# Performance work log

Measured on AMD Instinct MI355X. Metric: run time of the kernel, lower is better.

The kernel has to match this reference:

```python
import jax, jax.numpy as jnp
import numpy as np

B, S, D, H = 1, 2048, 4096, 32
HD = D // H  # 128


def setup_inputs() -> dict:
    key = jax.random.key(0)
    ks = jax.random.split(key, 6)
    x = jax.random.normal(ks[0], (B, S, D), dtype=jnp.float32)
    # rotary angles: standard llama freqs, position * inv_freq
    inv_freq = 1.0 / (10000.0 ** (jnp.arange(0, HD, 2, dtype=jnp.float32) / HD))  # (HD/2,)
    freqs = jnp.arange(S, dtype=jnp.float32)[:, None] * inv_freq[None, :]  # (S, HD/2)
    scale = 0.02
    wq = jax.random.normal(ks[1], (D, D), dtype=jnp.float32) * scale
    wk = jax.random.normal(ks[2], (D, D), dtype=jnp.float32) * scale
    wv = jax.random.normal(ks[3], (D, D), dtype=jnp.float32) * scale
    wo = jax.random.normal(ks[4], (D, D), dtype=jnp.float32) * scale
    return {"x": x, "freqs": freqs, "wq": wq, "wk": wk, "wv": wv, "wo": wo}


def _rope(t, cos, sin):
    # t: (B,S,H,HD); pairs are interleaved (complex view of last dim)
    b, s, h, d = t.shape
    t2 = t.reshape(b, s, h, d // 2, 2)
    t0, t1 = t2[..., 0], t2[..., 1]
    o0 = t0 * cos - t1 * sin
    o1 = t0 * sin + t1 * cos
    return jnp.stack([o0, o1], axis=-1).reshape(b, s, h, d)


def reference(x, freqs, wq, wk, wv, wo):
    b, s, d = x.shape
    hd = 2 * freqs.shape[-1]
    h = d // hd
    # projections (torch Linear: y = x @ W.T)
    q = (x @ wq.T).reshape(b, s, h, hd)
    k = (x @ wk.T).reshape(b, s, h, hd)
    v = (x @ wv.T).reshape(b, s, h, hd)
    cos = jnp.cos(freqs)[None, :s, None, :]  # (1,S,1,HD/2)
    sin = jnp.sin(freqs)[None, :s, None, :]
    q = _rope(q, cos, sin)
    k = _rope(k, cos, sin)
    q = q.transpose(0, 2, 1, 3)  # (B,H,S,HD)
    k = k.transpose(0, 2, 1, 3)
    v = v.transpose(0, 2, 1, 3)
    scale = jnp.sqrt(jnp.float32(hd))
    scores = jnp.einsum('bhqd,bhkd->bhqk', q, k).astype(jnp.float32) / scale
    # causal mask (qp == ep path): -inf strictly above diagonal
    mask = jnp.triu(jnp.full((s, s), -jnp.inf, dtype=scores.dtype), k=1)
    scores = scores + mask[None, None]
    attn = jax.nn.softmax(scores, axis=-1).astype(q.dtype)
    out = jnp.einsum('bhqk,bhkd->bhqd', attn, v)
    out = out.transpose(0, 2, 1, 3).reshape(b, s, d)
    return out @ wo.T
```

## Files before the change

kernel.cpp:

```cpp
#include <hip/hip_runtime.h>
#include <hip/hip_bf16.h>
#include <stdint.h>


typedef __attribute__((ext_vector_type(8))) short bf16x8;
typedef __attribute__((ext_vector_type(4))) float f32x4;

#define S_LEN 2048
#define DMODEL 4096
#define NHEAD 32
#define HDIM 128
#define QKV_LD 12288

__device__ __forceinline__ unsigned short f2bf(float f) {
  unsigned int u = __float_as_uint(f);
  unsigned int r = u + 0x7FFFu + ((u >> 16) & 1u);
  return (unsigned short)(r >> 16);
}
__device__ __forceinline__ float bf2f(unsigned short h) {
  return __uint_as_float(((unsigned int)h) << 16);
}
__device__ __forceinline__ void gl_lds16(const void* g, void* l) {
  __builtin_amdgcn_global_load_lds((const __attribute__((address_space(1))) unsigned int*)g,
                                   (__attribute__((address_space(3))) unsigned int*)l, 16, 0, 0);
}
__device__ __forceinline__ void phase_barrier() {
  __builtin_amdgcn_sched_barrier(0);
  asm volatile("" ::: "memory");
  __builtin_amdgcn_s_barrier();
  asm volatile("" ::: "memory");
  __builtin_amdgcn_sched_barrier(0);
}
__device__ __forceinline__ void wait_vmcnt6() {
  __builtin_amdgcn_sched_barrier(0);
  asm volatile("s_waitcnt vmcnt(6)" ::: "memory");
  __builtin_amdgcn_sched_barrier(0);
}
__device__ __forceinline__ void wait_vmcnt4() {
  __builtin_amdgcn_sched_barrier(0);
  asm volatile("s_waitcnt vmcnt(4)" ::: "memory");
  __builtin_amdgcn_sched_barrier(0);
}

__device__ __forceinline__ void cvt4(const float* __restrict__ s, unsigned short* __restrict__ d,
                                     int i) {
  float4 v = ((const float4*)s)[i];
  ushort4 o;
  o.x = f2bf(v.x); o.y = f2bf(v.y); o.z = f2bf(v.z); o.w = f2bf(v.w);
  ((ushort4*)d)[i] = o;
}

__global__ __launch_bounds__(256) void prep_inputs(const float* __restrict__ x,
                                                   const float* __restrict__ wq,
                                                   const float* __restrict__ wk,
                                                   const float* __restrict__ wv,
                                                   const float* __restrict__ wo,
                                                   const float* __restrict__ fr,
                                                   unsigned short* __restrict__ xb,
                                                   unsigned short* __restrict__ wqkvb,
                                                   unsigned short* __restrict__ wob,
                                                   float* __restrict__ cs) {
  const int NX = 2097152;
  const int NW = 4194304;
  const int NR = S_LEN * 64;
  const int total = NX + 4 * NW + NR;
  int i = blockIdx.x * blockDim.x + threadIdx.x;
  int stride = gridDim.x * blockDim.x;
  for (; i < total; i += stride) {
    if (i < NX) {
      cvt4(x, xb, i);
    } else if (i < NX + NW) {
      cvt4(wq, wqkvb, i - NX);
    } else if (i < NX + 2 * NW) {
      cvt4(wk, wqkvb + 16777216, i - NX - NW);
    } else if (i < NX + 3 * NW) {
      cvt4(wv, wqkvb + 33554432, i - NX - 2 * NW);
    } else if (i < NX + 4 * NW) {
      cvt4(wo, wob, i - NX - 3 * NW);
    } else {
      int j = i - (NX + 4 * NW);
      float f = fr[j];
      cs[2 * j]     = cosf(f);
      cs[2 * j + 1] = sinf(f);
    }
  }
}

__device__ __forceinline__ void mfma_quad(f32x4 (&acc)[8][4], const bf16x8 (&af)[4][2],
                                          const bf16x8 (&bf)[2][2], int moff, int noff) {
  __builtin_amdgcn_s_setprio(1);
#pragma unroll
  for (int mi = 0; mi < 4; ++mi)
#pragma unroll
    for (int ni = 0; ni < 2; ++ni)
#pragma unroll
      for (int kk = 0; kk < 2; ++kk)
        acc[moff + mi][noff + ni] = __builtin_amdgcn_mfma_f32_16x16x32_bf16(
            af[mi][kk], bf[ni][kk], acc[moff + mi][noff + ni], 0, 0, 0);
  __builtin_amdgcn_s_setprio(0);
}
__device__ __forceinline__ void mfma_quad2(f32x4 (&acc)[4][4], const bf16x8 (&af)[2][2],
                                           const bf16x8 (&bf)[2][2], int moff, int noff) {
  __builtin_amdgcn_s_setprio(1);
#pragma unroll
  for (int mi = 0; mi < 2; ++mi)
#pragma unroll
    for (int ni = 0; ni < 2; ++ni)
#pragma unroll
      for (int kk = 0; kk < 2; ++kk)
        acc[moff + mi][noff + ni] = __builtin_amdgcn_mfma_f32_16x16x32_bf16(
            af[mi][kk], bf[ni][kk], acc[moff + mi][noff + ni], 0, 0, 0);
  __builtin_amdgcn_s_setprio(0);
}

__device__ __forceinline__ void read_a(bf16x8 (&dst)[4][2], const char* base, int half,
                                       int wr, int l15, int l4, int swz) {
#pragma unroll
  for (int mi = 0; mi < 4; ++mi) {
    const char* rb = base + (wr * 128 + half * 64 + mi * 16 + l15) * 128;
#pragma unroll
    for (int kk = 0; kk < 2; ++kk)
      dst[mi][kk] = *(const bf16x8*)(rb + ((kk * 64 + l4 * 16) ^ swz));
  }
}
__device__ __forceinline__ void read_b(bf16x8 (&dst)[2][2], const char* base, int half,
                                       int wc, int l15, int l4, int swz) {
#pragma unroll
  for (int ni = 0; ni < 2; ++ni) {
    const char* rb = base + (wc * 64 + half * 32 + ni * 16 + l15) * 128;
#pragma unroll
    for (int kk = 0; kk < 2; ++kk)
      dst[ni][kk] = *(const bf16x8*)(rb + ((kk * 64 + l4 * 16) ^ swz));
  }
}
__device__ __forceinline__ void read_a2(bf16x8 (&dst)[2][2], const char* base, int half,
                                        int wr, int l15, int l4, int swz) {
#pragma unroll
  for (int mi = 0; mi < 2; ++mi) {
    const char* rb = base + (wr * 64 + half * 32 + mi * 16 + l15) * 128;
#pragma unroll
    for (int kk = 0; kk < 2; ++kk)
      dst[mi][kk] = *(const bf16x8*)(rb + ((kk * 64 + l4 * 16) ^ swz));
  }
}
__device__ __forceinline__ void read_b2(bf16x8 (&dst)[2][2], const char* base, int half,
                                        int wc, int l15, int l4, int swz) {
#pragma unroll
  for (int ni = 0; ni < 2; ++ni) {
    const char* rb = base + (wc * 64 + half * 32 + ni * 16 + l15) * 128;
#pragma unroll
    for (int kk = 0; kk < 2; ++kk)
      dst[ni][kk] = *(const bf16x8*)(rb + ((kk * 64 + l4 * 16) ^ swz));
  }
}

template <bool OUT_BF16, bool ROPE>
__device__ __forceinline__ void gemm256_body(const unsigned short* __restrict__ A,
                                             const unsigned short* __restrict__ B,
                                             void* __restrict__ C,
                                             int M, int N, int K, int ldc,
                                             char* smem, int wg,
                                             const float* __restrict__ cs) {
  const int tid = threadIdx.x;
  const int lane = tid & 63, wid = tid >> 6;
  const int wr = wid >> 2, wc = wid & 3;
  const int l15 = lane & 15, l4 = lane >> 4;

  const int nbn = N >> 8;
  const int bm = wg / nbn, bn = wg % nbn;
  const int nk = K >> 6;

  unsigned short* AlB = (unsigned short*)smem;
  unsigned short* BlB = (unsigned short*)smem + 32768;

  const int srow = tid >> 3;
  const int scol = ((tid & 7) ^ (srow & 7)) * 8;
  const unsigned short* Asrc = A + (size_t)(bm * 256 + srow) * K + scol;
  const unsigned short* Bsrc = B + (size_t)(bn * 256 + srow) * K + scol;
  const int ldsdst = wid * 512;

#define STA(b, kt, q) gl_lds16(Asrc + ((size_t)(q) * 64) * K + (kt) * 64, AlB + (b) * 16384 + (q) * 4096 + ldsdst)
#define STB(b, kt, q) gl_lds16(Bsrc + ((size_t)(q) * 64) * K + (kt) * 64, BlB + (b) * 16384 + (q) * 4096 + ldsdst)

  const int swz = (l15 & 7) << 4;

  f32x4 acc[8][4] = {};
  bf16x8 Ax[4][2], Ay[4][2], B0f[2][2], B1f[2][2];

#pragma unroll
  for (int q = 0; q < 4; ++q) STA(0, 0, q);
#pragma unroll
  for (int q = 0; q < 4; ++q) STB(0, 0, q);
  {
    const int k1 = (nk > 1) ? 1 : 0;
    STA(1, k1, 0); STA(1, k1, 2);
    STB(1, k1, 0); STB(1, k1, 1); STB(1, k1, 2); STB(1, k1, 3);
  }
  wait_vmcnt6();
  phase_barrier();
  read_a(Ax, (const char*)AlB, 0, wr, l15, l4, swz);
  read_b(B0f, (const char*)BlB, 0, wc, l15, l4, swz);

#define HALF(bb, AC, AA, t)                                                \
  {                                                                        \
    const int kt1 = ((t) + 1 < nk) ? (t) + 1 : nk - 1;                     \
    const int kt2 = ((t) + 2 < nk) ? (t) + 2 : nk - 1;                     \
    const char* Ab = (const char*)(AlB + (bb) * 16384);                    \
    const char* Bb = (const char*)(BlB + (bb) * 16384);                    \
    const char* Abn = (const char*)(AlB + ((bb) ^ 1) * 16384);             \
    const char* Bbn = (const char*)(BlB + ((bb) ^ 1) * 16384);             \
    STA((bb) ^ 1, kt1, 1); STA((bb) ^ 1, kt1, 3);                          \
    phase_barrier();                                                       \
    mfma_quad(acc, AC, B0f, 0, 0);                                 \
    read_a(AA, Ab, 1, wr, l15, l4, swz);                                   \
    STA(bb, kt2, 0); STA(bb, kt2, 2);                                      \
    phase_barrier();                                                       \
    mfma_quad(acc, AA, B0f, 4, 0);                                 \
    read_b(B1f, Bb, 1, wc, l15, l4, swz);                                  \
    STB(bb, kt2, 0); STB(bb, kt2, 1);                                      \
    phase_barrier();                                                       \
    mfma_quad(acc, AA, B1f, 4, 2);                                 \
    STB(bb, kt2, 2); STB(bb, kt2, 3);                                      \
    wait_vmcnt6();                                                         \
    phase_barrier();                                                       \
    mfma_quad(acc, AC, B1f, 0, 2);                                 \
    read_a(AA, Abn, 0, wr, l15, l4, swz);                                  \
    read_b(B0f, Bbn, 0, wc, l15, l4, swz);                                 \
  }

  for (int t = 0; t < nk; t += 2) {
    HALF(0, Ax, Ay, t);
    HALF(1, Ay, Ax, t + 1);
  }
#undef HALF
#undef STA
#undef STB

  __builtin_amdgcn_sched_barrier(0);
  asm volatile("s_waitcnt vmcnt(0)" ::: "memory");

  const size_t crow0 = (size_t)bm * 256 + wr * 128 + l4 * 4;
  const int ccol0 = bn * 256 + wc * 64 + l15;
#pragma unroll
  for (int mf = 0; mf < 8; ++mf)
#pragma unroll
    for (int nf = 0; nf < 4; ++nf) {
      size_t row = crow0 + mf * 16;
      int col = ccol0 + nf * 16;
      if (ROPE) {
        const int d = col & (HDIM - 1);
        const int i2 = d & ~1;
        unsigned short* Cp = (unsigned short*)C;
#pragma unroll
        for (int r = 0; r < 4; ++r) {
          float v = acc[mf][nf][r];
          float vp = __shfl_xor(v, 1, 64);
          float2 csv = *(const float2*)&cs[(row + r) * HDIM + i2];
          float o = ((d & 1) == 0) ? (v * csv.x - vp * csv.y)
                                   : (vp * csv.y + v * csv.x);
          Cp[(row + r) * ldc + col] = f2bf(o);
        }
      } else if (OUT_BF16) {
        unsigned short* Cp = (unsigned short*)C;
#pragma unroll
        for (int r = 0; r < 4; ++r) Cp[(row + r) * ldc + col] = f2bf(acc[mf][nf][r]);
      } else {
        float* Cp = (float*)C;
#pragma unroll
        for (int r = 0; r < 4; ++r) Cp[(row + r) * ldc + col] = acc[mf][nf][r];
      }
    }
}

template <bool OUT_BF16>
__device__ __forceinline__ void gemm128_body(const unsigned short* __restrict__ A,
                                             const unsigned short* __restrict__ B,
                                             void* __restrict__ C,
                                             int M, int N, int K, int ldc,
                                             char* smem, int wg) {
  const int tid = threadIdx.x;
  const int lane = tid & 63, wid = tid >> 6;
  const int wr = wid >> 2, wc = wid & 3;
  const int l15 = lane & 15, l4 = lane >> 4;

  const int nbn = N >> 8;
  const int bm = wg / nbn, bn = wg % nbn;
  const int nk = K >> 6;

  unsigned short* AlB = (unsigned short*)smem;
  unsigned short* BlB = (unsigned short*)smem + 16384;

  const int srow = tid >> 3;
  const int scol = ((tid & 7) ^ (srow & 7)) * 8;
  const unsigned short* Asrc = A + (size_t)(bm * 128 + srow) * K + scol;
  const unsigned short* Bsrc = B + (size_t)(bn * 256 + srow) * K + scol;
  const int ldsdst = wid * 512;

#define STA2(b, kt, q) gl_lds16(Asrc + ((size_t)(q) * 64) * K + (kt) * 64, AlB + (b) * 8192 + (q) * 4096 + ldsdst)
#define STB2(b, kt, q) gl_lds16(Bsrc + ((size_t)(q) * 64) * K + (kt) * 64, BlB + (b) * 16384 + (q) * 4096 + ldsdst)

  const int swz = (l15 & 7) << 4;

  f32x4 acc[4][4] = {};
  bf16x8 Ax[2][2], Ay[2][2], B0f[2][2], B1f[2][2];

  STA2(0, 0, 0); STA2(0, 0, 1);
#pragma unroll
  for (int q = 0; q < 4; ++q) STB2(0, 0, q);
  {
    const int k1 = (nk > 1) ? 1 : 0;
    STA2(1, k1, 0); STA2(1, k1, 1);
    STB2(1, k1, 0); STB2(1, k1, 1);
  }
  wait_vmcnt4();
  phase_barrier();
  read_a2(Ax, (const char*)AlB, 0, wr, l15, l4, swz);
  read_b2(B0f, (const char*)BlB, 0, wc, l15, l4, swz);

#define HALF2(bb, AC, AA, t)                                               \
  {                                                                        \
    const int kt1 = ((t) + 1 < nk) ? (t) + 1 : nk - 1;                     \
    const int kt2 = ((t) + 2 < nk) ? (t) + 2 : nk - 1;                     \
    const char* Ab = (const char*)(AlB + (bb) * 8192);                     \
    const char* Bb = (const char*)(BlB + (bb) * 16384);                    \
    const char* Abn = (const char*)(AlB + ((bb) ^ 1) * 8192);              \
    const char* Bbn = (const char*)(BlB + ((bb) ^ 1) * 16384);             \
    STB2((bb) ^ 1, kt1, 2); STB2((bb) ^ 1, kt1, 3);        \
    phase_barrier();                                                       \
    mfma_quad2(acc, AC, B0f, 0, 0);                                \
    read_a2(AA, Ab, 1, wr, l15, l4, swz);                                  \
    STA2(bb, kt2, 0); STA2(bb, kt2, 1);                                    \
    phase_barrier();                                                       \
    mfma_quad2(acc, AA, B0f, 2, 0);                                \
    read_b2(B1f, Bb, 1, wc, l15, l4, swz);                                 \
    STB2(bb, kt2, 0); STB2(bb, kt2, 1);                                    \
    phase_barrier();                                                       \
    mfma_quad2(acc, AA, B1f, 2, 2);                                \
    wait_vmcnt4();                                                         \
    phase_barrier();                                                       \
    mfma_quad2(acc, AC, B1f, 0, 2);                                \
    read_a2(AA, Abn, 0, wr, l15, l4, swz);                                 \
    read_b2(B0f, Bbn, 0, wc, l15, l4, swz);                                \
  }

  for (int t = 0; t < nk; t += 2) {
    HALF2(0, Ax, Ay, t);
    HALF2(1, Ay, Ax, t + 1);
  }
#undef HALF2
#undef STA2
#undef STB2

  __builtin_amdgcn_sched_barrier(0);
  asm volatile("s_waitcnt vmcnt(0)" ::: "memory");

  const size_t crow0 = (size_t)bm * 128 + wr * 64 + l4 * 4;
  const int ccol0 = bn * 256 + wc * 64 + l15;
#pragma unroll
  for (int mf = 0; mf < 4; ++mf)
#pragma unroll
    for (int nf = 0; nf < 4; ++nf) {
      size_t row = crow0 + mf * 16;
      int col = ccol0 + nf * 16;
      if (OUT_BF16) {
        unsigned short* Cp = (unsigned short*)C;
#pragma unroll
        for (int r = 0; r < 4; ++r) Cp[(row + r) * ldc + col] = f2bf(acc[mf][nf][r]);
      } else {
        float* Cp = (float*)C;
#pragma unroll
        for (int r = 0; r < 4; ++r) Cp[(row + r) * ldc + col] = acc[mf][nf][r];
      }
    }
}

__global__ __launch_bounds__(512, 2) void qkv_proj(const unsigned short* __restrict__ xb,
                                                   const unsigned short* __restrict__ wqkvb,
                                                   unsigned short* __restrict__ qkvb,
                                                   const float* __restrict__ cs) {
  __shared__ __align__(16) char smem[131072];
  const int b = blockIdx.x;
  if (b < 256) {
    gemm256_body<true, true>(xb, wqkvb, qkvb, 2048, 8192, 4096, QKV_LD, smem, b, cs);
  } else {
    gemm128_body<true>(xb, wqkvb + 33554432, qkvb + 8192, 2048, 4096, 4096, QKV_LD, smem, b - 256);
  }
}

__global__ __launch_bounds__(512, 2) void out_proj(const unsigned short* __restrict__ A,
                                                   const unsigned short* __restrict__ B,
                                                   float* __restrict__ C) {
  __shared__ __align__(16) char smem[98304];
  gemm128_body<false>(A, B, C, 2048, 4096, 4096, 4096, smem, blockIdx.x);
}

__global__ __launch_bounds__(256) void v_transpose(const unsigned short* __restrict__ qkv,
                                                   unsigned short* __restrict__ vt) {
  __shared__ unsigned short T[64][68];
  int sb = blockIdx.x * 64;
  int h = blockIdx.y >> 1;
  int d0 = (blockIdx.y & 1) * 64;
  int tid = threadIdx.x;
#pragma unroll
  for (int i = 0; i < 2; ++i) {
    int b = i * 256 + tid;
    int r = b >> 3, c = b & 7;
    const ushort4* src = (const ushort4*)(qkv + (size_t)(sb + r) * QKV_LD + 8192 + h * HDIM + d0 + c * 8);
    ushort4 a0 = src[0], a1 = src[1];
    *(ushort4*)&T[r][c * 8] = a0;
    *(ushort4*)&T[r][c * 8 + 4] = a1;
  }
  __syncthreads();
#pragma unroll
  for (int i = 0; i < 2; ++i) {
    int b = i * 256 + tid;
    int dd = b >> 3, sc = b & 7;
    unsigned short tmp[8];
#pragma unroll
    for (int j = 0; j < 8; ++j) tmp[j] = T[sc * 8 + j][dd];
    unsigned short* dst = vt + (size_t)(h * HDIM + d0 + dd) * S_LEN + sb + sc * 8;
    ushort4 lo = make_ushort4(tmp[0], tmp[1], tmp[2], tmp[3]);
    ushort4 hi = make_ushort4(tmp[4], tmp[5], tmp[6], tmp[7]);
    *(ushort4*)dst = lo;
    *(ushort4*)(dst + 4) = hi;
  }
}

__global__ __launch_bounds__(256) void attn_kernel(const unsigned short* __restrict__ qkv,
                                                   const unsigned short* __restrict__ vt,
                                                   float* __restrict__ pacc,
                                                   float* __restrict__ pm,
                                                   float* __restrict__ pl) {
  __shared__ __align__(16) unsigned short Klds[64 * 128];
  __shared__ __align__(16) unsigned short Vtlds[128 * 64];
  __shared__ __align__(16) unsigned short Plds[4][16 * 64];
  const int tid = threadIdx.x, lane = tid & 63, w = tid >> 6;
  const int l15 = lane & 15, l4 = lane >> 4;
  const int h = blockIdx.x & 31;
  const int jj = blockIdx.x >> 5;

  int bq, c, kt0, kt1;
  if (jj < 17) {
    bq = 31 - jj; c = 0; kt0 = 0; kt1 = 16;
  } else {
    int k = jj - 17;
    if (k == 0)      { bq = 31;            c = 1; }
    else if (k & 1)  { bq = 30 - (k >> 1); c = 1; }
    else             { bq = 15 - (k >> 1); c = 0; }
    kt0 = c ? 16 : 0;
    kt1 = bq + 1;
  }
  const int qw = bq * 64 + w * 16;

  bf16x8 qf[4];
#pragma unroll
  for (int ds = 0; ds < 4; ++ds)
    qf[ds] = *(const bf16x8*)&qkv[(size_t)(qw + l15) * QKV_LD + h * HDIM + ds * 32 + l4 * 8];

  f32x4 acc[8] = {};
  float m_run[4], l_run[4];
#pragma unroll
  for (int r = 0; r < 4; ++r) { m_run[r] = -1e30f; l_run[r] = 0.f; }

  const float scale = 0.08838834764831845f;
  for (int kt = kt0; kt < kt1; ++kt) {
    const int kv0 = kt * 64;
    __syncthreads();
#pragma unroll
    for (int i = 0; i < 4; ++i) {
      int b = (w * 4 + i) * 64 + lane;
      int r = b >> 4, cc = b & 15;
      gl_lds16(qkv + (size_t)(kv0 + r) * QKV_LD + 4096 + h * HDIM + ((cc ^ (r & 15)) * 8),
               &Klds[(w * 4 + i) * 512]);
    }
#pragma unroll
    for (int i = 0; i < 4; ++i) {
      int b = (w * 4 + i) * 64 + lane;
      int r = b >> 3, cc = b & 7;
      gl_lds16(vt + (size_t)(h * HDIM + r) * S_LEN + kv0 + ((cc ^ (r & 7)) * 8),
               &Vtlds[(w * 4 + i) * 512]);
    }
    __syncthreads();

    f32x4 s[4] = {};
#pragma unroll
    for (int jt = 0; jt < 4; ++jt) {
      int kr = jt * 16 + l15;
#pragma unroll
      for (int ds = 0; ds < 4; ++ds) {
        int cc = (ds * 4 + l4) ^ (kr & 15);
        bf16x8 kf = *(const bf16x8*)&Klds[kr * 128 + cc * 8];
        s[jt] = __builtin_amdgcn_mfma_f32_16x16x32_bf16(qf[ds], kf, s[jt], 0, 0, 0);
      }
    }

    const bool diag = (kt == bq);
#pragma unroll
    for (int jt = 0; jt < 4; ++jt)
#pragma unroll
      for (int r = 0; r < 4; ++r) {
        float v = s[jt][r] * scale;
        if (diag) {
          int kvg = kv0 + jt * 16 + l15;
          int qg = qw + l4 * 4 + r;
          if (kvg > qg) v = -1e30f;
        }
        s[jt][r] = v;
      }

    float alpha[4];
#pragma unroll
    for (int r = 0; r < 4; ++r) {
      float mx = fmaxf(fmaxf(s[0][r], s[1][r]), fmaxf(s[2][r], s[3][r]));
#pragma unroll
      for (int off = 1; off < 16; off <<= 1) mx = fmaxf(mx, __shfl_xor(mx, off, 64));
      float mi = fmaxf(m_run[r], mx);
      alpha[r] = __expf(m_run[r] - mi);
      m_run[r] = mi;
      float sum = 0.f;
#pragma unroll
      for (int jt = 0; jt < 4; ++jt) {
        float p = __expf(s[jt][r] - mi);
        s[jt][r] = p;
        sum += p;
      }
#pragma unroll
      for (int off = 1; off < 16; off <<= 1) sum += __shfl_xor(sum, off, 64);
      l_run[r] = l_run[r] * alpha[r] + sum;
    }
#pragma unroll
    for (int dt = 0; dt < 8; ++dt)
#pragma unroll
      for (int r = 0; r < 4; ++r) acc[dt][r] *= alpha[r];

    unsigned short* P = &Plds[w][0];
#pragma unroll
    for (int jt = 0; jt < 4; ++jt)
#pragma unroll
      for (int r = 0; r < 4; ++r) {
        int row = l4 * 4 + r, col = jt * 16 + l15;
        P[(row * 64 + col) ^ ((row & 7) << 3)] = f2bf(s[jt][r]);
      }

#pragma unroll
    for (int ks = 0; ks < 2; ++ks) {
      bf16x8 pa = *(const bf16x8*)&P[(l15 * 64 + ks * 32 + l4 * 8) ^ ((l15 & 7) << 3)];
#pragma unroll
      for (int dt = 0; dt < 8; ++dt) {
        int vr = dt * 16 + l15;
        int cc = (ks * 4 + l4) ^ (vr & 7);
        bf16x8 vf = *(const bf16x8*)&Vtlds[vr * 64 + cc * 8];
        acc[dt] = __builtin_amdgcn_mfma_f32_16x16x32_bf16(pa, vf, acc[dt], 0, 0, 0);
      }
    }
  }

  const size_t bj = ((size_t)h * 32 + bq) * 2 + c;
  float* pa = pacc + bj * 8192 + (size_t)(w * 16) * 128;
#pragma unroll
  for (int dt = 0; dt < 8; ++dt)
#pragma unroll
    for (int r = 0; r < 4; ++r)
      pa[(l4 * 4 + r) * 128 + dt * 16 + l15] = acc[dt][r];
  if (l15 == 0) {
#pragma unroll
    for (int r = 0; r < 4; ++r) {
      pm[bj * 64 + w * 16 + l4 * 4 + r] = m_run[r];
      pl[bj * 64 + w * 16 + l4 * 4 + r] = l_run[r];
    }
  }
}

__global__ __launch_bounds__(256) void attn_combine(const float* __restrict__ pacc,
                                                    const float* __restrict__ pm,
                                                    const float* __restrict__ pl,
                                                    unsigned short* __restrict__ out) {
  const int x = blockIdx.x;
  const int bq = x >> 5, h = x & 31;
  const int tid = threadIdx.x;
  const int row = tid >> 2;
  const int d0 = (tid & 3) * 32;
  const size_t base = ((size_t)h * 32 + bq) * 2;
  const float m0 = pm[base * 64 + row];
  const float l0 = pl[base * 64 + row];
  const int nc = (bq >= 16) ? 2 : 1;
  float w0 = 1.f, w1 = 0.f, denom = l0;
  if (nc == 2) {
    float m1 = pm[(base + 1) * 64 + row];
    float l1 = pl[(base + 1) * 64 + row];
    float M = fmaxf(m0, m1);
    w0 = __expf(m0 - M);
    w1 = __expf(m1 - M);
    denom = w0 * l0 + w1 * l1;
  }
  const float inv = 1.f / denom;
  const float* a0 = pacc + base * 8192 + row * 128 + d0;
  const float* a1 = a0 + 8192;
  unsigned short* op = out + (size_t)(bq * 64 + row) * DMODEL + h * HDIM + d0;
#pragma unroll
  for (int i = 0; i < 8; ++i) {
    float4 v = *(const float4*)(a0 + i * 4);
    v.x *= w0; v.y *= w0; v.z *= w0; v.w *= w0;
    if (nc == 2) {
      float4 u = *(const float4*)(a1 + i * 4);
      v.x += w1 * u.x; v.y += w1 * u.y; v.z += w1 * u.z; v.w += w1 * u.w;
    }
    ushort4 o;
    o.x = f2bf(v.x * inv); o.y = f2bf(v.y * inv);
    o.z = f2bf(v.z * inv); o.w = f2bf(v.w * inv);
    *(ushort4*)(op + i * 4) = o;
  }
}

extern "C" void kernel_launch(void* const* d_in, const int* in_sizes, int n_in,
                              void* d_out, int out_size, void* d_ws, size_t ws_size,
                              hipStream_t stream) {
  const float* x = (const float*)d_in[0];
  const float* fr = (const float*)d_in[1];
  const float* wq = (const float*)d_in[2];
  const float* wk = (const float*)d_in[3];
  const float* wv = (const float*)d_in[4];
  const float* wo = (const float*)d_in[5];

  char* ws = (char*)d_ws;
  const size_t OFF_XB   = 0;
  const size_t OFF_WQKV = 16777216;
  const size_t OFF_WO   = OFF_WQKV + 100663296;
  const size_t OFF_QKV  = OFF_WO + 33554432;
  const size_t OFF_CS   = OFF_QKV + 50331648;
  const size_t OFF_VT   = OFF_CS + 1048576;
  const size_t OFF_ATTN = OFF_VT + 16777216;

  unsigned short* xb    = (unsigned short*)(ws + OFF_XB);
  unsigned short* wqkvb = (unsigned short*)(ws + OFF_WQKV);
  unsigned short* wob   = (unsigned short*)(ws + OFF_WO);
  unsigned short* qkvb  = (unsigned short*)(ws + OFF_QKV);
  float*          cs    = (float*)(ws + OFF_CS);
  unsigned short* vt    = (unsigned short*)(ws + OFF_VT);
  unsigned short* attn  = (unsigned short*)(ws + OFF_ATTN);
  float* pacc = (float*)(ws + OFF_WQKV);
  float* pm   = (float*)(ws + OFF_WQKV + 67108864);
  float* pl   = (float*)(ws + OFF_WQKV + 67633152);

  prep_inputs<<<2048, 256, 0, stream>>>(x, wq, wk, wv, wo, fr, xb, wqkvb, wob, cs);
  qkv_proj<<<dim3(512), 512, 0, stream>>>(xb, wqkvb, qkvb, cs);
  v_transpose<<<dim3(32, 64), 256, 0, stream>>>(qkvb, vt);
  attn_kernel<<<dim3(1536), 256, 0, stream>>>(qkvb, vt, pacc, pm, pl);
  attn_combine<<<dim3(1024), 256, 0, stream>>>(pacc, pm, pl, attn);
  out_proj<<<dim3(256), 512, 0, stream>>>(attn, wob, (float*)d_out);
}
```

Before: 477.6 us.

## Double-buffer K/V tiles in attention with async prefetch two tiles ahead

Splits the K and Vt shared-memory tiles into two buffers and issues the global-to-LDS loads for tile kt+2 right after finishing compute on tile kt. The loop now waits with vmcnt(8) instead of two full __syncthreads, so load latency can overlap with the MFMA work. This doubles LDS use to about 72KB per block, which may reduce occupancy, and at the end of the range it issues redundant loads of the last tile.

Result: no change. 480.0 us (+0.5%).

```diff
diff --git a/kernel.cpp b/kernel.cpp
--- a/kernel.cpp
+++ b/kernel.cpp
@@ -39,6 +39,11 @@
 __device__ __forceinline__ void wait_vmcnt4() {
   __builtin_amdgcn_sched_barrier(0);
   asm volatile("s_waitcnt vmcnt(4)" ::: "memory");
+  __builtin_amdgcn_sched_barrier(0);
+}
+__device__ __forceinline__ void wait_vmcnt8() {
+  __builtin_amdgcn_sched_barrier(0);
+  asm volatile("s_waitcnt vmcnt(8)" ::: "memory");
   __builtin_amdgcn_sched_barrier(0);
 }
 
@@ -431,8 +436,8 @@
                                                    float* __restrict__ pacc,
                                                    float* __restrict__ pm,
                                                    float* __restrict__ pl) {
-  __shared__ __align__(16) unsigned short Klds[64 * 128];
-  __shared__ __align__(16) unsigned short Vtlds[128 * 64];
+  __shared__ __align__(16) unsigned short Klds[2][64 * 128];
+  __shared__ __align__(16) unsigned short Vtlds[2][128 * 64];
   __shared__ __align__(16) unsigned short Plds[4][16 * 64];
   const int tid = threadIdx.x, lane = tid & 63, w = tid >> 6;
   const int l15 = lane & 15, l4 = lane >> 4;
@@ -462,25 +467,36 @@
 #pragma unroll
   for (int r = 0; r < 4; ++r) { m_run[r] = -1e30f; l_run[r] = 0.f; }
 
+#define STAGE_KV(kt, bi)                                                            \
+  {                                                                                 \
+    const int kv0s = (kt) * 64;                                                     \
+    _Pragma("unroll") for (int i = 0; i < 4; ++i) {                                 \
+      int b2 = (w * 4 + i) * 64 + lane;                                             \
+      int r = b2 >> 4, cc = b2 & 15;                                                \
+      gl_lds16(qkv + (size_t)(kv0s + r) * QKV_LD + 4096 + h * HDIM +                \
+                   ((cc ^ (r & 15)) * 8),                                           \
+               &Klds[bi][(w * 4 + i) * 512]);                                       \
+    }                                                                               \
+    _Pragma("unroll") for (int i = 0; i < 4; ++i) {                                 \
+      int b2 = (w * 4 + i) * 64 + lane;                                             \
+      int r = b2 >> 3, cc = b2 & 7;                                                 \
+      gl_lds16(vt + (size_t)(h * HDIM + r) * S_LEN + kv0s + ((cc ^ (r & 7)) * 8),   \
+               &Vtlds[bi][(w * 4 + i) * 512]);                                      \
+    }                                                                               \
+  }
+
   const float scale = 0.08838834764831845f;
+  STAGE_KV(kt0, 0);
+  {
+    const int t1 = (kt0 + 1 < kt1) ? kt0 + 1 : kt1 - 1;
+    STAGE_KV(t1, 1);
+  }
+
   for (int kt = kt0; kt < kt1; ++kt) {
+    const int bufi = (kt - kt0) & 1;
     const int kv0 = kt * 64;
-    __syncthreads();
-#pragma unroll
-    for (int i = 0; i < 4; ++i) {
-      int b = (w * 4 + i) * 64 + lane;
-      int r = b >> 4, cc = b & 15;
-      gl_lds16(qkv + (size_t)(kv0 + r) * QKV_LD + 4096 + h * HDIM + ((cc ^ (r & 15)) * 8),
-               &Klds[(w * 4 + i) * 512]);
-    }
-#pragma unroll
-    for (int i = 0; i < 4; ++i) {
-      int b = (w * 4 + i) * 64 + lane;
-      int r = b >> 3, cc = b & 7;
-      gl_lds16(vt + (size_t)(h * HDIM + r) * S_LEN + kv0 + ((cc ^ (r & 7)) * 8),
-               &Vtlds[(w * 4 + i) * 512]);
-    }
-    __syncthreads();
+    wait_vmcnt8();
+    phase_barrier();
 
     f32x4 s[4] = {};
 #pragma unroll
@@ -489,7 +505,7 @@
 #pragma unroll
       for (int ds = 0; ds < 4; ++ds) {
         int cc = (ds * 4 + l4) ^ (kr & 15);
-        bf16x8 kf = *(const bf16x8*)&Klds[kr * 128 + cc * 8];
+        bf16x8 kf = *(const bf16x8*)&Klds[bufi][kr * 128 + cc * 8];
         s[jt] = __builtin_amdgcn_mfma_f32_16x16x32_bf16(qf[ds], kf, s[jt], 0, 0, 0);
       }
     }
@@ -549,11 +565,18 @@
       for (int dt = 0; dt < 8; ++dt) {
         int vr = dt * 16 + l15;
         int cc = (ks * 4 + l4) ^ (vr & 7);
-        bf16x8 vf = *(const bf16x8*)&Vtlds[vr * 64 + cc * 8];
+        bf16x8 vf = *(const bf16x8*)&Vtlds[bufi][vr * 64 + cc * 8];
         acc[dt] = __builtin_amdgcn_mfma_f32_16x16x32_bf16(pa, vf, acc[dt], 0, 0, 0);
       }
     }
-  }
+
+    phase_barrier();
+    {
+      const int tn = (kt + 2 < kt1) ? kt + 2 : kt1 - 1;
+      STAGE_KV(tn, bufi);
+    }
+  }
+#undef STAGE_KV
 
   const size_t bj = ((size_t)h * 32 + bq) * 2 + c;
   float* pa = pacc + bj * 8192 + (size_t)(w * 16) * 128;
```

## Fuse V transpose into QKV GEMM epilogue, fold softmax scale, skip combine for unsplit rows

Applied to the files above, without the earlier changes.

The V projection GEMM now writes its output already transposed through a shared-memory staging tile, which removes the separate v_transpose kernel and its extra round trip of V through global memory. The softmax scale times log2(e) is folded into Q during the RoPE epilogue, so attention uses exp2 and drops the per-score multiply. Query blocks that are not split across two KV chunks write their normalised output directly, so the combine kernel runs only on the split half and launches half as many blocks. The transpose epilogue adds LDS traffic and a barrier to the GEMM, and the folded scale slightly changes the rounding of Q in bf16.

After: 414.4 us. 1.15x faster.

```diff
diff --git a/kernel.cpp b/kernel.cpp
--- a/kernel.cpp
+++ b/kernel.cpp
@@ -11,6 +11,8 @@
 #define NHEAD 32
 #define HDIM 128
 #define QKV_LD 12288
+
+#define QSCALE 0.1275247584969759f
 
 __device__ __forceinline__ unsigned short f2bf(float f) {
   unsigned int u = __float_as_uint(f);
@@ -250,6 +252,7 @@
       if (ROPE) {
         const int d = col & (HDIM - 1);
         const int i2 = d & ~1;
+        const float fs = (col < 4096) ? QSCALE : 1.0f;
         unsigned short* Cp = (unsigned short*)C;
 #pragma unroll
         for (int r = 0; r < 4; ++r) {
@@ -258,7 +261,7 @@
           float2 csv = *(const float2*)&cs[(row + r) * HDIM + i2];
           float o = ((d & 1) == 0) ? (v * csv.x - vp * csv.y)
                                    : (vp * csv.y + v * csv.x);
-          Cp[(row + r) * ldc + col] = f2bf(o);
+          Cp[(row + r) * ldc + col] = f2bf(o * fs);
         }
       } else if (OUT_BF16) {
         unsigned short* Cp = (unsigned short*)C;
@@ -272,7 +275,7 @@
     }
 }
 
-template <bool OUT_BF16>
+template <bool OUT_BF16, bool VT_OUT>
 __device__ __forceinline__ void gemm128_body(const unsigned short* __restrict__ A,
                                              const unsigned short* __restrict__ B,
                                              void* __restrict__ C,
@@ -354,6 +357,36 @@
   __builtin_amdgcn_sched_barrier(0);
   asm volatile("s_waitcnt vmcnt(0)" ::: "memory");
 
+  if (VT_OUT) {
+    unsigned short* Tw = (unsigned short*)smem + (size_t)wid * 4672;
+#pragma unroll
+    for (int mf = 0; mf < 4; ++mf)
+#pragma unroll
+      for (int nf = 0; nf < 4; ++nf)
+#pragma unroll
+        for (int r = 0; r < 4; ++r) {
+          int lr = mf * 16 + l4 * 4 + r;
+          int lc = nf * 16 + l15;
+          Tw[lr * 73 + lc] = f2bf(acc[mf][nf][r]);
+        }
+    __syncthreads();
+    unsigned short* vtp = (unsigned short*)C;
+    const int gcol0 = bn * 256 + wc * 64;
+    const int grow0 = bm * 128 + wr * 64;
+    const int dl8 = lane >> 3, sc = lane & 7;
+#pragma unroll
+    for (int it = 0; it < 8; ++it) {
+      int dl = it * 8 + dl8;
+      unsigned short tmp[8];
+#pragma unroll
+      for (int j = 0; j < 8; ++j) tmp[j] = Tw[(sc * 8 + j) * 73 + dl];
+      unsigned short* dst = vtp + (size_t)(gcol0 + dl) * S_LEN + grow0 + sc * 8;
+      *(ushort4*)dst = make_ushort4(tmp[0], tmp[1], tmp[2], tmp[3]);
+      *(ushort4*)(dst + 4) = make_ushort4(tmp[4], tmp[5], tmp[6], tmp[7]);
+    }
+    return;
+  }
+
   const size_t crow0 = (size_t)bm * 128 + wr * 64 + l4 * 4;
   const int ccol0 = bn * 256 + wc * 64 + l15;
 #pragma unroll
@@ -377,13 +410,14 @@
 __global__ __launch_bounds__(512, 2) void qkv_proj(const unsigned short* __restrict__ xb,
                                                    const unsigned short* __restrict__ wqkvb,
                                                    unsigned short* __restrict__ qkvb,
+                                                   unsigned short* __restrict__ vt,
                                                    const float* __restrict__ cs) {
   __shared__ __align__(16) char smem[131072];
   const int b = blockIdx.x;
   if (b < 256) {
     gemm256_body<true, true>(xb, wqkvb, qkvb, 2048, 8192, 4096, QKV_LD, smem, b, cs);
   } else {
-    gemm128_body<true>(xb, wqkvb + 33554432, qkvb + 8192, 2048, 4096, 4096, QKV_LD, smem, b - 256);
+    gemm128_body<true, true>(xb, wqkvb + 33554432, vt, 2048, 4096, 4096, 0, smem, b - 256);
   }
 }
 
@@ -391,46 +425,15 @@
                                                    const unsigned short* __restrict__ B,
                                                    float* __restrict__ C) {
   __shared__ __align__(16) char smem[98304];
-  gemm128_body<false>(A, B, C, 2048, 4096, 4096, 4096, smem, blockIdx.x);
-}
-
-__global__ __launch_bounds__(256) void v_transpose(const unsigned short* __restrict__ qkv,
-                                                   unsigned short* __restrict__ vt) {
-  __shared__ unsigned short T[64][68];
-  int sb = blockIdx.x * 64;
-  int h = blockIdx.y >> 1;
-  int d0 = (blockIdx.y & 1) * 64;
-  int tid = threadIdx.x;
-#pragma unroll
-  for (int i = 0; i < 2; ++i) {
-    int b = i * 256 + tid;
-    int r = b >> 3, c = b & 7;
-    const ushort4* src = (const ushort4*)(qkv + (size_t)(sb + r) * QKV_LD + 8192 + h * HDIM + d0 + c * 8);
-    ushort4 a0 = src[0], a1 = src[1];
-    *(ushort4*)&T[r][c * 8] = a0;
-    *(ushort4*)&T[r][c * 8 + 4] = a1;
-  }
-  __syncthreads();
-#pragma unroll
-  for (int i = 0; i < 2; ++i) {
-    int b = i * 256 + tid;
-    int dd = b >> 3, sc = b & 7;
-    unsigned short tmp[8];
-#pragma unroll
-    for (int j = 0; j < 8; ++j) tmp[j] = T[sc * 8 + j][dd];
-    unsigned short* dst = vt + (size_t)(h * HDIM + d0 + dd) * S_LEN + sb + sc * 8;
-    ushort4 lo = make_ushort4(tmp[0], tmp[1], tmp[2], tmp[3]);
-    ushort4 hi = make_ushort4(tmp[4], tmp[5], tmp[6], tmp[7]);
-    *(ushort4*)dst = lo;
-    *(ushort4*)(dst + 4) = hi;
-  }
+  gemm128_body<false, false>(A, B, C, 2048, 4096, 4096, 4096, smem, blockIdx.x);
 }
 
 __global__ __launch_bounds__(256) void attn_kernel(const unsigned short* __restrict__ qkv,
                                                    const unsigned short* __restrict__ vt,
                                                    float* __restrict__ pacc,
                                                    float* __restrict__ pm,
-                                                   float* __restrict__ pl) {
+                                                   float* __restrict__ pl,
+                                                   unsigned short* __restrict__ out) {
   __shared__ __align__(16) unsigned short Klds[64 * 128];
   __shared__ __align__(16) unsigned short Vtlds[128 * 64];
   __shared__ __align__(16) unsigned short Plds[4][16 * 64];
@@ -450,6 +453,7 @@
     kt0 = c ? 16 : 0;
     kt1 = bq + 1;
   }
+  if (jj == 16) kt1 = 16;
   const int qw = bq * 64 + w * 16;
 
   bf16x8 qf[4];
@@ -462,7 +466,6 @@
 #pragma unroll
   for (int r = 0; r < 4; ++r) { m_run[r] = -1e30f; l_run[r] = 0.f; }
 
-  const float scale = 0.08838834764831845f;
   for (int kt = kt0; kt < kt1; ++kt) {
     const int kv0 = kt * 64;
     __syncthreads();
@@ -495,18 +498,16 @@
     }
 
     const bool diag = (kt == bq);
-#pragma unroll
-    for (int jt = 0; jt < 4; ++jt)
-#pragma unroll
-      for (int r = 0; r < 4; ++r) {
-        float v = s[jt][r] * scale;
-        if (diag) {
+    if (diag) {
+#pragma unroll
+      for (int jt = 0; jt < 4; ++jt)
+#pragma unroll
+        for (int r = 0; r < 4; ++r) {
           int kvg = kv0 + jt * 16 + l15;
           int qg = qw + l4 * 4 + r;
-          if (kvg > qg) v = -1e30f;
+          if (kvg > qg) s[jt][r] = -1e30f;
         }
-        s[jt][r] = v;
-      }
+    }
 
     float alpha[4];
 #pragma unroll
@@ -515,12 +516,12 @@
 #pragma unroll
       for (int off = 1; off < 16; off <<= 1) mx = fmaxf(mx, __shfl_xor(mx, off, 64));
       float mi = fmaxf(m_run[r], mx);
-      alpha[r] = __expf(m_run[r] - mi);
+      alpha[r] = exp2f(m_run[r] - mi);
       m_run[r] = mi;
       float sum = 0.f;
 #pragma unroll
       for (int jt = 0; jt < 4; ++jt) {
-        float p = __expf(s[jt][r] - mi);
+        float p = exp2f(s[jt][r] - mi);
         s[jt][r] = p;
         sum += p;
       }
@@ -555,18 +556,32 @@
     }
   }
 
-  const size_t bj = ((size_t)h * 32 + bq) * 2 + c;
-  float* pa = pacc + bj * 8192 + (size_t)(w * 16) * 128;
-#pragma unroll
-  for (int dt = 0; dt < 8; ++dt)
-#pragma unroll
-    for (int r = 0; r < 4; ++r)
-      pa[(l4 * 4 + r) * 128 + dt * 16 + l15] = acc[dt][r];
-  if (l15 == 0) {
-#pragma unroll
-    for (int r = 0; r < 4; ++r) {
-      pm[bj * 64 + w * 16 + l4 * 4 + r] = m_run[r];
-      pl[bj * 64 + w * 16 + l4 * 4 + r] = l_run[r];
+  if (bq < 16) {
+    float inv[4];
+#pragma unroll
+    for (int r = 0; r < 4; ++r) inv[r] = 1.f / l_run[r];
+#pragma unroll
+    for (int dt = 0; dt < 8; ++dt)
+#pragma unroll
+      for (int r = 0; r < 4; ++r) {
+        int row = qw + l4 * 4 + r;
+        int col = h * HDIM + dt * 16 + l15;
+        out[(size_t)row * DMODEL + col] = f2bf(acc[dt][r] * inv[r]);
+      }
+  } else {
+    const size_t bj = ((size_t)h * 32 + bq) * 2 + c;
+    float* pa = pacc + bj * 8192 + (size_t)(w * 16) * 128;
+#pragma unroll
+    for (int dt = 0; dt < 8; ++dt)
+#pragma unroll
+      for (int r = 0; r < 4; ++r)
+        pa[(l4 * 4 + r) * 128 + dt * 16 + l15] = acc[dt][r];
+    if (l15 == 0) {
+#pragma unroll
+      for (int r = 0; r < 4; ++r) {
+        pm[bj * 64 + w * 16 + l4 * 4 + r] = m_run[r];
+        pl[bj * 64 + w * 16 + l4 * 4 + r] = l_run[r];
+      }
     }
   }
 }
@@ -576,23 +591,19 @@
                                                     const float* __restrict__ pl,
                                                     unsigned short* __restrict__ out) {
   const int x = blockIdx.x;
-  const int bq = x >> 5, h = x & 31;
+  const int bq = 16 + (x >> 5), h = x & 31;
   const int tid = threadIdx.x;
   const int row = tid >> 2;
   const int d0 = (tid & 3) * 32;
   const size_t base = ((size_t)h * 32 + bq) * 2;
   const float m0 = pm[base * 64 + row];
   const float l0 = pl[base * 64 + row];
-  const int nc = (bq >= 16) ? 2 : 1;
-  float w0 = 1.f, w1 = 0.f, denom = l0;
-  if (nc == 2) {
-    float m1 = pm[(base + 1) * 64 + row];
-    float l1 = pl[(base + 1) * 64 + row];
-    float M = fmaxf(m0, m1);
-    w0 = __expf(m0 - M);
-    w1 = __expf(m1 - M);
-    denom = w0 * l0 + w1 * l1;
-  }
+  float m1 = pm[(base + 1) * 64 + row];
+  float l1 = pl[(base + 1) * 64 + row];
+  float M = fmaxf(m0, m1);
+  float w0 = exp2f(m0 - M);
+  float w1 = exp2f(m1 - M);
+  float denom = w0 * l0 + w1 * l1;
   const float inv = 1.f / denom;
   const float* a0 = pacc + base * 8192 + row * 128 + d0;
   const float* a1 = a0 + 8192;
@@ -600,14 +611,12 @@
 #pragma unroll
   for (int i = 0; i < 8; ++i) {
     float4 v = *(const float4*)(a0 + i * 4);
-    v.x *= w0; v.y *= w0; v.z *= w0; v.w *= w0;
-    if (nc == 2) {
-      float4 u = *(const float4*)(a1 + i * 4);
-      v.x += w1 * u.x; v.y += w1 * u.y; v.z += w1 * u.z; v.w += w1 * u.w;
-    }
+    float4 u = *(const float4*)(a1 + i * 4);
     ushort4 o;
-    o.x = f2bf(v.x * inv); o.y = f2bf(v.y * inv);
-    o.z = f2bf(v.z * inv); o.w = f2bf(v.w * inv);
+    o.x = f2bf((w0 * v.x + w1 * u.x) * inv);
+    o.y = f2bf((w0 * v.y + w1 * u.y) * inv);
+    o.z = f2bf((w0 * v.z + w1 * u.z) * inv);
+    o.w = f2bf((w0 * v.w + w1 * u.w) * inv);
     *(ushort4*)(op + i * 4) = o;
   }
 }
@@ -643,9 +652,8 @@
   float* pl   = (float*)(ws + OFF_WQKV + 67633152);
 
   prep_inputs<<<2048, 256, 0, stream>>>(x, wq, wk, wv, wo, fr, xb, wqkvb, wob, cs);
-  qkv_proj<<<dim3(512), 512, 0, stream>>>(xb, wqkvb, qkvb, cs);
-  v_transpose<<<dim3(32, 64), 256, 0, stream>>>(qkvb, vt);
-  attn_kernel<<<dim3(1536), 256, 0, stream>>>(qkvb, vt, pacc, pm, pl);
-  attn_combine<<<dim3(1024), 256, 0, stream>>>(pacc, pm, pl, attn);
+  qkv_proj<<<dim3(512), 512, 0, stream>>>(xb, wqkvb, qkvb, vt, cs);
+  attn_kernel<<<dim3(1536), 256, 0, stream>>>(qkvb, vt, pacc, pm, pl, attn);
+  attn_combine<<<dim3(512), 256, 0, stream>>>(pacc, pm, pl, attn);
   out_proj<<<dim3(256), 512, 0, stream>>>(attn, wob, (float*)d_out);
 }
```
